# Performance work log

Measured on AMD Instinct MI355X. Metric: run time of the kernel, lower is better.

Reference implementation:

```python
import jax, jax.numpy as jnp
import numpy as np

B, T, D = 8, 8192, 768

def setup_inputs() -> dict:
    key = jax.random.key(0)
    k1, k2 = jax.random.split(key)
    x = jax.random.normal(k1, (B, T, D), dtype=jnp.float32)
    stimulus = jax.random.normal(k2, (B, T, D), dtype=jnp.float32)
    return {"x": x, "stimulus": stimulus}

def reference(x, stimulus):
    # Per-position dot product: out[b, t] = sum_d x[b, t, d] * stimulus[b, t, d]
    return jnp.einsum("btd,btd->bt", x, stimulus)
```

## Files before the change

kernel.cpp:

```cpp
#include <hip/hip_runtime.h>


constexpr int D = 768;
constexpr int D4 = D / 4;
constexpr int ROWS = 8 * 8192;

__global__ __launch_bounds__(256) void row_dot_kernel(
    const float4* __restrict__ x,
    const float4* __restrict__ s,
    float* __restrict__ out)
{
    const int wave = (blockIdx.x * blockDim.x + threadIdx.x) >> 6;
    const int lane = threadIdx.x & 63;
    if (wave >= ROWS) return;

    const size_t base = (size_t)wave * D4;

    float acc = 0.0f;
#pragma unroll
    for (int c = 0; c < 3; ++c) {
        float4 a = x[base + c * 64 + lane];
        float4 b = s[base + c * 64 + lane];
        acc = fmaf(a.x, b.x, acc);
        acc = fmaf(a.y, b.y, acc);
        acc = fmaf(a.z, b.z, acc);
        acc = fmaf(a.w, b.w, acc);
    }

#pragma unroll
    for (int off = 32; off > 0; off >>= 1)
        acc += __shfl_down(acc, off, 64);

    if (lane == 0) out[wave] = acc;
}

extern "C" void kernel_launch(void* const* d_in, const int* in_sizes, int n_in,
                              void* d_out, int out_size, void* d_ws, size_t ws_size,
                              hipStream_t stream)
{
    const float4* x = (const float4*)d_in[0];
    const float4* s = (const float4*)d_in[1];
    float* out = (float*)d_out;

    const int waves_per_block = 4;
    const int blocks = ROWS / waves_per_block;
    row_dot_kernel<<<blocks, 256, 0, stream>>>(x, s, out);
}
```

Baseline: 382.2 us.

## Use persistent grid-stride waves processing four rows each with batched loads

Replaces one-wave-per-row launch with a fixed grid of 1024 blocks whose waves loop over the rows, four consecutive rows per iteration. All 24 float4 loads for those rows are issued before the FMAs, raising memory-level parallelism per wave. Results for the four rows are written with a single float4 store. It trades occupancy (fewer resident waves) for more in-flight loads per wave.

```diff
diff --git a/kernel.cpp b/kernel.cpp
--- a/kernel.cpp
+++ b/kernel.cpp
@@ -1,37 +1,60 @@
 #include <hip/hip_runtime.h>
 
 
-constexpr int D = 768;
-constexpr int D4 = D / 4;
-constexpr int ROWS = 8 * 8192;
+constexpr int D4    = 768 / 4;
+constexpr int ROWS  = 8 * 8192;
+constexpr int RPI   = 4;
+constexpr int TPB   = 256;
+constexpr int BLOCKS = 1024;
+constexpr int NWAVES = BLOCKS * TPB / 64;
 
-__global__ __launch_bounds__(256) void row_dot_kernel(
+__global__ __launch_bounds__(TPB) void row_dot_kernel(
     const float4* __restrict__ x,
-    const float4* __restrict__ s,
+    const float4* __restrict__ y,
     float* __restrict__ out)
 {
-    const int wave = (blockIdx.x * blockDim.x + threadIdx.x) >> 6;
+    const int wave = blockIdx.x * (TPB / 64) + (threadIdx.x >> 6);
     const int lane = threadIdx.x & 63;
-    if (wave >= ROWS) return;
 
-    const size_t base = (size_t)wave * D4;
+    for (int r0 = wave * RPI; r0 < ROWS; r0 += NWAVES * RPI) {
+        const size_t b = (size_t)r0 * D4 + lane;
 
-    float acc = 0.0f;
+        float acc0 = 0.f, acc1 = 0.f, acc2 = 0.f, acc3 = 0.f;
 #pragma unroll
-    for (int c = 0; c < 3; ++c) {
-        float4 a = x[base + c * 64 + lane];
-        float4 b = s[base + c * 64 + lane];
-        acc = fmaf(a.x, b.x, acc);
-        acc = fmaf(a.y, b.y, acc);
-        acc = fmaf(a.z, b.z, acc);
-        acc = fmaf(a.w, b.w, acc);
-    }
+        for (int c = 0; c < 3; ++c) {
+            const size_t o = b + c * 64;
+            float4 a0 = x[o];
+            float4 a1 = x[o + 1 * D4];
+            float4 a2 = x[o + 2 * D4];
+            float4 a3 = x[o + 3 * D4];
+            float4 s0 = y[o];
+            float4 s1 = y[o + 1 * D4];
+            float4 s2 = y[o + 2 * D4];
+            float4 s3 = y[o + 3 * D4];
+
+            acc0 = fmaf(a0.x, s0.x, acc0); acc0 = fmaf(a0.y, s0.y, acc0);
+            acc0 = fmaf(a0.z, s0.z, acc0); acc0 = fmaf(a0.w, s0.w, acc0);
+            acc1 = fmaf(a1.x, s1.x, acc1); acc1 = fmaf(a1.y, s1.y, acc1);
+            acc1 = fmaf(a1.z, s1.z, acc1); acc1 = fmaf(a1.w, s1.w, acc1);
+            acc2 = fmaf(a2.x, s2.x, acc2); acc2 = fmaf(a2.y, s2.y, acc2);
+            acc2 = fmaf(a2.z, s2.z, acc2); acc2 = fmaf(a2.w, s2.w, acc2);
+            acc3 = fmaf(a3.x, s3.x, acc3); acc3 = fmaf(a3.y, s3.y, acc3);
+            acc3 = fmaf(a3.z, s3.z, acc3); acc3 = fmaf(a3.w, s3.w, acc3);
+        }
 
 #pragma unroll
-    for (int off = 32; off > 0; off >>= 1)
-        acc += __shfl_down(acc, off, 64);
+        for (int off = 32; off > 0; off >>= 1) {
+            acc0 += __shfl_down(acc0, off, 64);
+            acc1 += __shfl_down(acc1, off, 64);
+            acc2 += __shfl_down(acc2, off, 64);
+            acc3 += __shfl_down(acc3, off, 64);
+        }
 
-    if (lane == 0) out[wave] = acc;
+        if (lane == 0) {
+            *reinterpret_cast<float4*>(out + r0) =
+                make_float4(acc0, acc1, acc2, acc3);
+        }
+    }
 }
 
 extern "C" void kernel_launch(void* const* d_in, const int* in_sizes, int n_in,
@@ -39,10 +62,8 @@
                               hipStream_t stream)
 {
     const float4* x = (const float4*)d_in[0];
-    const float4* s = (const float4*)d_in[1];
+    const float4* y = (const float4*)d_in[1];
     float* out = (float*)d_out;
 
-    const int waves_per_block = 4;
-    const int blocks = ROWS / waves_per_block;
-    row_dot_kernel<<<blocks, 256, 0, stream>>>(x, s, out);
+    row_dot_kernel<<<BLOCKS, TPB, 0, stream>>>(x, y, out);
 }
```

Result: no change. 387.2 us (+1.3%).
